# Kernel tuning notes

Measured on AMD Instinct MI355X. Metric: run time of the kernel, lower is better.

Reference implementation:

```python
import math
import jax, jax.numpy as jnp
import numpy as np
from jax import lax

FS = 16000.0
TAU_FAST_MS = 2.0
TAU_SLOW_MS = 60.0
EPS = 1e-6


def setup_inputs() -> dict:
    key = jax.random.key(0)
    B, C, T = 8, 64, 64000
    x = jax.random.normal(key, (B, C, T), dtype=jnp.float32)
    mu_fast = jnp.float32(1.0 - math.exp(-1.0 / (FS * TAU_FAST_MS / 1000.0)))
    mu_slow = jnp.float32(1.0 - math.exp(-1.0 / (FS * TAU_SLOW_MS / 1000.0)))
    mix_weight_adapt = jnp.float32(0.5)
    mix_weight_hp = jnp.float32(0.3)
    return {
        "x": x,
        "mu_fast": mu_fast,
        "mu_slow": mu_slow,
        "mix_weight_adapt": mix_weight_adapt,
        "mix_weight_hp": mix_weight_hp,
    }


def reference(x, mu_fast, mu_slow, mix_weight_adapt, mix_weight_hp):
    # x: [B, C, T]
    x = jnp.maximum(x, 0.0)
    xt = jnp.moveaxis(x, -1, 0)  # [T, B, C], time-leading for scan

    def step(carry, xcur):
        mf, ms = carry
        mf = (1.0 - mu_fast) * mf + mu_fast * xcur
        ms = (1.0 - mu_slow) * ms + mu_slow * xcur
        return (mf, ms), (mf, ms)

    init = (xt[0], xt[0])  # EMA initialized at first sample
    _, (mf_rest, ms_rest) = lax.scan(step, init, xt[1:])
    M_fast = jnp.concatenate([xt[:1], mf_rest], axis=0)  # [T, B, C]
    M_slow = jnp.concatenate([xt[:1], ms_rest], axis=0)

    mix_adapt = jax.nn.sigmoid(mix_weight_adapt)
    M = mix_adapt * M_fast + (1.0 - mix_adapt) * M_slow
    M = jnp.moveaxis(M, 0, -1)  # back to [B, C, T]

    x_adapted = x / (EPS + M)
    x_hp = x - M
    mix_hp = jax.nn.sigmoid(mix_weight_hp)
    return x_adapted + mix_hp * x_hp
```

## Files before the change

kernel.cpp:

```cpp
#include <hip/hip_runtime.h>


#define THREADS 128
#define WPB 2
#define K 25
#define WTILE (64 * K)
#define NBUF 3
#define T_LEN 64000
#define SEGS_W 4
#define SEG_LEN (T_LEN / SEGS_W)
#define SEG_TILES (SEG_LEN / WTILE)
#define HALO_TILES 4
#define EPS_V 1e-6f

typedef float nfloat4 __attribute__((ext_vector_type(4)));

__device__ __forceinline__ float rfl(float v) {
    return __int_as_float(__builtin_amdgcn_readfirstlane(__float_as_int(v)));
}

__device__ __forceinline__ void stage(const float* gt, float* b, int lane) {
#pragma unroll
    for (int c = 0; c < 6; ++c)
        __builtin_amdgcn_global_load_lds(
            (const __attribute__((address_space(1))) unsigned int*)(gt + c * 256 + lane * 4),
            (__attribute__((address_space(3))) unsigned int*)(b + c * 256),
            16, 0, 0);
    __builtin_amdgcn_global_load_lds(
        (const __attribute__((address_space(1))) unsigned int*)(gt + 1536 + lane),
        (__attribute__((address_space(3))) unsigned int*)(b + 1536),
        4, 0, 0);
}

__global__ __launch_bounds__(THREADS, 2)
void dual_ema_hp_kernel(const float* __restrict__ x,
                        const float* __restrict__ p_mu_fast,
                        const float* __restrict__ p_mu_slow,
                        const float* __restrict__ p_mwa,
                        const float* __restrict__ p_mhp,
                        float* __restrict__ out)
{
    __shared__ __align__(16) float lds[WPB * NBUF * WTILE];
    const int tid  = threadIdx.x;
    const int lane = tid & 63;
    const int wv   = tid >> 6;
    float* bufs = &lds[wv * NBUF * WTILE];

    const int gw  = blockIdx.x * WPB + wv;
    const int row = gw / SEGS_W;
    const int seg = gw % SEGS_W;
    const int h   = (seg == 0) ? 0 : HALO_TILES;
    const int nt  = SEG_TILES + h;

    const float* gseg = x   + (size_t)row * T_LEN + (size_t)seg * SEG_LEN - (size_t)h * WTILE;
    float*       oseg = out + (size_t)row * T_LEN + (size_t)seg * SEG_LEN - (size_t)h * WTILE;

    const float mu_f = rfl(p_mu_fast[0]);
    const float mu_s = rfl(p_mu_slow[0]);
    const float af = rfl(1.0f - mu_f);
    const float as = rfl(1.0f - mu_s);
    const float wa  = rfl(1.0f / (1.0f + __expf(-p_mwa[0])));
    const float wb  = rfl(1.0f - wa);
    const float whp = rfl(1.0f / (1.0f + __expf(-p_mhp[0])));

    const float Pf1  = rfl(__powf(af, (float)K));
    const float Ps1  = rfl(__powf(as, (float)K));
    const float Pf2  = rfl(Pf1 * Pf1),   Ps2  = rfl(Ps1 * Ps1);
    const float Pf4  = rfl(Pf2 * Pf2),   Ps4  = rfl(Ps2 * Ps2);
    const float Pf8  = rfl(Pf4 * Pf4),   Ps8  = rfl(Ps4 * Ps4);
    const float Pf16 = rfl(Pf8 * Pf8),   Ps16 = rfl(Ps8 * Ps8);
    const float Pf32 = rfl(Pf16 * Pf16), Ps32 = rfl(Ps16 * Ps16);

    stage(gseg,         bufs + 0 * WTILE, lane);
    stage(gseg + WTILE, bufs + 1 * WTILE, lane);

    float sfr = 0.0f, ssr = 0.0f;

    for (int t = 0; t < nt; ++t) {
        float* buf = bufs + (t % NBUF) * WTILE;

        if (t > h && t < nt - 1) { asm volatile("s_waitcnt vmcnt(14)" ::: "memory"); }
        else                     { asm volatile("s_waitcnt vmcnt(7)"  ::: "memory"); }

        if (t + 2 < nt)
            stage(gseg + (size_t)(t + 2) * WTILE, bufs + ((t + 2) % NBUF) * WTILE, lane);

        if (seg == 0 && t == 0 && lane == 0) {
            float y0 = fmaxf(buf[0], 0.0f);
            sfr = y0; ssr = y0;
        }

        float inf = (lane == 0) ? sfr : 0.0f;
        float ins = (lane == 0) ? ssr : 0.0f;
        float mf, ms;
        {
            float yv = fmaxf(buf[lane * K], 0.0f);
            mf = fmaf(af, inf, mu_f * yv);
            ms = fmaf(as, ins, mu_s * yv);
        }
#pragma unroll
        for (int i = 1; i < K; ++i) {
            float yv = fmaxf(buf[lane * K + i], 0.0f);
            mf = fmaf(af, mf, mu_f * yv);
            ms = fmaf(as, ms, mu_s * yv);
        }

        float cf = mf, cs = ms, uf, us;
        uf = __shfl_up(cf, 1);  us = __shfl_up(cs, 1);
        cf = (lane >= 1)  ? fmaf(Pf1,  uf, cf) : cf;  cs = (lane >= 1)  ? fmaf(Ps1,  us, cs) : cs;
        uf = __shfl_up(cf, 2);  us = __shfl_up(cs, 2);
        cf = (lane >= 2)  ? fmaf(Pf2,  uf, cf) : cf;  cs = (lane >= 2)  ? fmaf(Ps2,  us, cs) : cs;
        uf = __shfl_up(cf, 4);  us = __shfl_up(cs, 4);
        cf = (lane >= 4)  ? fmaf(Pf4,  uf, cf) : cf;  cs = (lane >= 4)  ? fmaf(Ps4,  us, cs) : cs;
        uf = __shfl_up(cf, 8);  us = __shfl_up(cs, 8);
        cf = (lane >= 8)  ? fmaf(Pf8,  uf, cf) : cf;  cs = (lane >= 8)  ? fmaf(Ps8,  us, cs) : cs;
        uf = __shfl_up(cf, 16); us = __shfl_up(cs, 16);
        cf = (lane >= 16) ? fmaf(Pf16, uf, cf) : cf;  cs = (lane >= 16) ? fmaf(Ps16, us, cs) : cs;
        uf = __shfl_up(cf, 32); us = __shfl_up(cs, 32);
        cf = (lane >= 32) ? fmaf(Pf32, uf, cf) : cf;  cs = (lane >= 32) ? fmaf(Ps32, us, cs) : cs;

        float ex_f = __shfl_up(cf, 1), ex_s = __shfl_up(cs, 1);
        if (lane == 0) { ex_f = sfr; ex_s = ssr; }
        sfr = __shfl(cf, 63);
        ssr = __shfl(cs, 63);

        asm volatile("s_waitcnt lgkmcnt(0)" ::: "memory");

        const bool emit = (t >= h);
        if (emit) {
            float mf2 = ex_f, ms2 = ex_s;
#pragma unroll
            for (int i = 0; i < K; ++i) {
                float yv = fmaxf(buf[lane * K + i], 0.0f);
                mf2 = fmaf(af, mf2, mu_f * yv);
                ms2 = fmaf(as, ms2, mu_s * yv);
                float M = fmaf(wa, mf2, wb * ms2);
                float o = yv * __builtin_amdgcn_rcpf(EPS_V + M) + whp * (yv - M);
                buf[lane * K + i] = o;
            }
            asm volatile("s_waitcnt lgkmcnt(0)" ::: "memory");

            float* gout = oseg + (size_t)t * WTILE;
            nfloat4* go4 = (nfloat4*)gout;
            const nfloat4* o4 = (const nfloat4*)buf;
#pragma unroll
            for (int c = 0; c < 6; ++c) {
                nfloat4 v = o4[c * 64 + lane];
                __builtin_nontemporal_store(v, &go4[c * 64 + lane]);
            }
            __builtin_nontemporal_store(buf[1536 + lane], &gout[1536 + lane]);
        }
    }
}

extern "C" void kernel_launch(void* const* d_in, const int* in_sizes, int n_in,
                              void* d_out, int out_size, void* d_ws, size_t ws_size,
                              hipStream_t stream) {
    const float* x    = (const float*)d_in[0];
    const float* mu_f = (const float*)d_in[1];
    const float* mu_s = (const float*)d_in[2];
    const float* mwa  = (const float*)d_in[3];
    const float* mhp  = (const float*)d_in[4];
    float* out = (float*)d_out;

    const int rows   = in_sizes[0] / T_LEN;
    const int blocks = rows * SEGS_W / WPB;
    dual_ema_hp_kernel<<<blocks, THREADS, 0, stream>>>(x, mu_f, mu_s, mwa, mhp, out);
}
```

Before: 249.5 us.

## Replace LDS-staged tiles with register-prefetched float4 scan over more segments

The LDS triple-buffer staging via global_load_lds is removed. Each lane now holds 4 consecutive samples in registers, and a 5-deep rotating register prefetch loads vectorised float4 directly from global memory. The wave scan now runs per 256-sample tile, and rows are split into 10 segments with a 25-tile halo, giving more waves and 256-thread blocks. This cuts LDS traffic and serial per-lane work and raises parallelism, at the cost of one shuffle scan per 256 samples instead of per 1600 and more redundant halo reads.

```diff
diff --git a/kernel.cpp b/kernel.cpp
--- a/kernel.cpp
+++ b/kernel.cpp
@@ -1,16 +1,15 @@
 #include <hip/hip_runtime.h>
 
 
-#define THREADS 128
-#define WPB 2
-#define K 25
-#define WTILE (64 * K)
-#define NBUF 3
+#define THREADS 256
+#define WPB 4
+#define MTILE 256
 #define T_LEN 64000
-#define SEGS_W 4
+#define SEGS_W 10
 #define SEG_LEN (T_LEN / SEGS_W)
-#define SEG_TILES (SEG_LEN / WTILE)
-#define HALO_TILES 4
+#define SEG_MT (SEG_LEN / MTILE)
+#define HALO_MT 25
+#define D 5
 #define EPS_V 1e-6f
 
 typedef float nfloat4 __attribute__((ext_vector_type(4)));
@@ -19,20 +18,7 @@
     return __int_as_float(__builtin_amdgcn_readfirstlane(__float_as_int(v)));
 }
 
-__device__ __forceinline__ void stage(const float* gt, float* b, int lane) {
-#pragma unroll
-    for (int c = 0; c < 6; ++c)
-        __builtin_amdgcn_global_load_lds(
-            (const __attribute__((address_space(1))) unsigned int*)(gt + c * 256 + lane * 4),
-            (__attribute__((address_space(3))) unsigned int*)(b + c * 256),
-            16, 0, 0);
-    __builtin_amdgcn_global_load_lds(
-        (const __attribute__((address_space(1))) unsigned int*)(gt + 1536 + lane),
-        (__attribute__((address_space(3))) unsigned int*)(b + 1536),
-        4, 0, 0);
-}
-
-__global__ __launch_bounds__(THREADS, 2)
+__global__ __launch_bounds__(THREADS, 5)
 void dual_ema_hp_kernel(const float* __restrict__ x,
                         const float* __restrict__ p_mu_fast,
                         const float* __restrict__ p_mu_slow,
@@ -40,20 +26,20 @@
                         const float* __restrict__ p_mhp,
                         float* __restrict__ out)
 {
-    __shared__ __align__(16) float lds[WPB * NBUF * WTILE];
     const int tid  = threadIdx.x;
     const int lane = tid & 63;
     const int wv   = tid >> 6;
-    float* bufs = &lds[wv * NBUF * WTILE];
 
     const int gw  = blockIdx.x * WPB + wv;
     const int row = gw / SEGS_W;
     const int seg = gw % SEGS_W;
-    const int h   = (seg == 0) ? 0 : HALO_TILES;
-    const int nt  = SEG_TILES + h;
+    const int h   = (seg == 0) ? 0 : HALO_MT;
+    const int total = SEG_MT + h;
 
-    const float* gseg = x   + (size_t)row * T_LEN + (size_t)seg * SEG_LEN - (size_t)h * WTILE;
-    float*       oseg = out + (size_t)row * T_LEN + (size_t)seg * SEG_LEN - (size_t)h * WTILE;
+    const float* gseg = x   + (size_t)row * T_LEN + (size_t)seg * SEG_LEN - (size_t)h * MTILE;
+    float*       oseg = out + (size_t)row * T_LEN + (size_t)seg * SEG_LEN - (size_t)h * MTILE;
+    const nfloat4* g4 = (const nfloat4*)gseg;
+    nfloat4*      go4 = (nfloat4*)oseg;
 
     const float mu_f = rfl(p_mu_fast[0]);
     const float mu_s = rfl(p_mu_slow[0]);
@@ -63,94 +49,82 @@
     const float wb  = rfl(1.0f - wa);
     const float whp = rfl(1.0f / (1.0f + __expf(-p_mhp[0])));
 
-    const float Pf1  = rfl(__powf(af, (float)K));
-    const float Ps1  = rfl(__powf(as, (float)K));
-    const float Pf2  = rfl(Pf1 * Pf1),   Ps2  = rfl(Ps1 * Ps1);
-    const float Pf4  = rfl(Pf2 * Pf2),   Ps4  = rfl(Ps2 * Ps2);
-    const float Pf8  = rfl(Pf4 * Pf4),   Ps8  = rfl(Ps4 * Ps4);
-    const float Pf16 = rfl(Pf8 * Pf8),   Ps16 = rfl(Ps8 * Ps8);
-    const float Pf32 = rfl(Pf16 * Pf16), Ps32 = rfl(Ps16 * Ps16);
-
-    stage(gseg,         bufs + 0 * WTILE, lane);
-    stage(gseg + WTILE, bufs + 1 * WTILE, lane);
+    const float af2 = af * af,  as2 = as * as;
+    const float Pf1  = rfl(af2 * af2),      Ps1  = rfl(as2 * as2);
+    const float Pf2  = rfl(Pf1 * Pf1),      Ps2  = rfl(Ps1 * Ps1);
+    const float Pf4  = rfl(Pf2 * Pf2),      Ps4  = rfl(Ps2 * Ps2);
+    const float Pf8  = rfl(Pf4 * Pf4),      Ps8  = rfl(Ps4 * Ps4);
+    const float Pf16 = rfl(Pf8 * Pf8),      Ps16 = rfl(Ps8 * Ps8);
+    const float Pf32 = rfl(Pf16 * Pf16),    Ps32 = rfl(Ps16 * Ps16);
 
     float sfr = 0.0f, ssr = 0.0f;
 
-    for (int t = 0; t < nt; ++t) {
-        float* buf = bufs + (t % NBUF) * WTILE;
+    nfloat4 r0 = g4[0 * 64 + lane];
+    nfloat4 r1 = g4[1 * 64 + lane];
+    nfloat4 r2 = g4[2 * 64 + lane];
+    nfloat4 r3 = g4[3 * 64 + lane];
+    nfloat4 r4 = g4[4 * 64 + lane];
 
-        if (t > h && t < nt - 1) { asm volatile("s_waitcnt vmcnt(14)" ::: "memory"); }
-        else                     { asm volatile("s_waitcnt vmcnt(7)"  ::: "memory"); }
+#define BODY(T_, RB_) do {                                                        \
+    nfloat4 v = RB_;                                                              \
+    if ((T_) + D < total) RB_ = g4[((T_) + D) * 64 + lane];                       \
+    float y0 = fmaxf(v.x, 0.0f), y1 = fmaxf(v.y, 0.0f);                           \
+    float y2 = fmaxf(v.z, 0.0f), y3 = fmaxf(v.w, 0.0f);                           \
+    if (seg == 0 && (T_) == 0 && lane == 0) { sfr = y0; ssr = y0; }               \
+    float inf = (lane == 0) ? sfr : 0.0f;                                         \
+    float ins = (lane == 0) ? ssr : 0.0f;                                         \
+    float mf = fmaf(af, inf, mu_f * y0);  float ms = fmaf(as, ins, mu_s * y0);    \
+    mf = fmaf(af, mf, mu_f * y1);         ms = fmaf(as, ms, mu_s * y1);           \
+    mf = fmaf(af, mf, mu_f * y2);         ms = fmaf(as, ms, mu_s * y2);           \
+    mf = fmaf(af, mf, mu_f * y3);         ms = fmaf(as, ms, mu_s * y3);           \
+    float cf = mf, cs = ms, uf, us;                                               \
+    uf = __shfl_up(cf, 1);  us = __shfl_up(cs, 1);                                \
+    cf = (lane >= 1)  ? fmaf(Pf1,  uf, cf) : cf;                                  \
+    cs = (lane >= 1)  ? fmaf(Ps1,  us, cs) : cs;                                  \
+    uf = __shfl_up(cf, 2);  us = __shfl_up(cs, 2);                                \
+    cf = (lane >= 2)  ? fmaf(Pf2,  uf, cf) : cf;                                  \
+    cs = (lane >= 2)  ? fmaf(Ps2,  us, cs) : cs;                                  \
+    uf = __shfl_up(cf, 4);  us = __shfl_up(cs, 4);                                \
+    cf = (lane >= 4)  ? fmaf(Pf4,  uf, cf) : cf;                                  \
+    cs = (lane >= 4)  ? fmaf(Ps4,  us, cs) : cs;                                  \
+    uf = __shfl_up(cf, 8);  us = __shfl_up(cs, 8);                                \
+    cf = (lane >= 8)  ? fmaf(Pf8,  uf, cf) : cf;                                  \
+    cs = (lane >= 8)  ? fmaf(Ps8,  us, cs) : cs;                                  \
+    uf = __shfl_up(cf, 16); us = __shfl_up(cs, 16);                               \
+    cf = (lane >= 16) ? fmaf(Pf16, uf, cf) : cf;                                  \
+    cs = (lane >= 16) ? fmaf(Ps16, us, cs) : cs;                                  \
+    uf = __shfl_up(cf, 32); us = __shfl_up(cs, 32);                               \
+    cf = (lane >= 32) ? fmaf(Pf32, uf, cf) : cf;                                  \
+    cs = (lane >= 32) ? fmaf(Ps32, us, cs) : cs;                                  \
+    float ex_f = __shfl_up(cf, 1), ex_s = __shfl_up(cs, 1);                       \
+    if (lane == 0) { ex_f = sfr; ex_s = ssr; }                                    \
+    sfr = __shfl(cf, 63); ssr = __shfl(cs, 63);                                   \
+    if ((T_) >= h) {                                                              \
+        float mf2 = ex_f, ms2 = ex_s; nfloat4 o;                                  \
+        mf2 = fmaf(af, mf2, mu_f * y0); ms2 = fmaf(as, ms2, mu_s * y0);           \
+        { float M = fmaf(wa, mf2, wb * ms2);                                      \
+          o.x = y0 * __builtin_amdgcn_rcpf(EPS_V + M) + whp * (y0 - M); }         \
+        mf2 = fmaf(af, mf2, mu_f * y1); ms2 = fmaf(as, ms2, mu_s * y1);           \
+        { float M = fmaf(wa, mf2, wb * ms2);                                      \
+          o.y = y1 * __builtin_amdgcn_rcpf(EPS_V + M) + whp * (y1 - M); }         \
+        mf2 = fmaf(af, mf2, mu_f * y2); ms2 = fmaf(as, ms2, mu_s * y2);           \
+        { float M = fmaf(wa, mf2, wb * ms2);                                      \
+          o.z = y2 * __builtin_amdgcn_rcpf(EPS_V + M) + whp * (y2 - M); }         \
+        mf2 = fmaf(af, mf2, mu_f * y3); ms2 = fmaf(as, ms2, mu_s * y3);           \
+        { float M = fmaf(wa, mf2, wb * ms2);                                      \
+          o.w = y3 * __builtin_amdgcn_rcpf(EPS_V + M) + whp * (y3 - M); }         \
+        __builtin_nontemporal_store(o, &go4[(T_) * 64 + lane]);                   \
+    }                                                                             \
+} while (0)
 
-        if (t + 2 < nt)
-            stage(gseg + (size_t)(t + 2) * WTILE, bufs + ((t + 2) % NBUF) * WTILE, lane);
-
-        if (seg == 0 && t == 0 && lane == 0) {
-            float y0 = fmaxf(buf[0], 0.0f);
-            sfr = y0; ssr = y0;
-        }
-
-        float inf = (lane == 0) ? sfr : 0.0f;
-        float ins = (lane == 0) ? ssr : 0.0f;
-        float mf, ms;
-        {
-            float yv = fmaxf(buf[lane * K], 0.0f);
-            mf = fmaf(af, inf, mu_f * yv);
-            ms = fmaf(as, ins, mu_s * yv);
-        }
-#pragma unroll
-        for (int i = 1; i < K; ++i) {
-            float yv = fmaxf(buf[lane * K + i], 0.0f);
-            mf = fmaf(af, mf, mu_f * yv);
-            ms = fmaf(as, ms, mu_s * yv);
-        }
-
-        float cf = mf, cs = ms, uf, us;
-        uf = __shfl_up(cf, 1);  us = __shfl_up(cs, 1);
-        cf = (lane >= 1)  ? fmaf(Pf1,  uf, cf) : cf;  cs = (lane >= 1)  ? fmaf(Ps1,  us, cs) : cs;
-        uf = __shfl_up(cf, 2);  us = __shfl_up(cs, 2);
-        cf = (lane >= 2)  ? fmaf(Pf2,  uf, cf) : cf;  cs = (lane >= 2)  ? fmaf(Ps2,  us, cs) : cs;
-        uf = __shfl_up(cf, 4);  us = __shfl_up(cs, 4);
-        cf = (lane >= 4)  ? fmaf(Pf4,  uf, cf) : cf;  cs = (lane >= 4)  ? fmaf(Ps4,  us, cs) : cs;
-        uf = __shfl_up(cf, 8);  us = __shfl_up(cs, 8);
-        cf = (lane >= 8)  ? fmaf(Pf8,  uf, cf) : cf;  cs = (lane >= 8)  ? fmaf(Ps8,  us, cs) : cs;
-        uf = __shfl_up(cf, 16); us = __shfl_up(cs, 16);
-        cf = (lane >= 16) ? fmaf(Pf16, uf, cf) : cf;  cs = (lane >= 16) ? fmaf(Ps16, us, cs) : cs;
-        uf = __shfl_up(cf, 32); us = __shfl_up(cs, 32);
-        cf = (lane >= 32) ? fmaf(Pf32, uf, cf) : cf;  cs = (lane >= 32) ? fmaf(Ps32, us, cs) : cs;
-
-        float ex_f = __shfl_up(cf, 1), ex_s = __shfl_up(cs, 1);
-        if (lane == 0) { ex_f = sfr; ex_s = ssr; }
-        sfr = __shfl(cf, 63);
-        ssr = __shfl(cs, 63);
-
-        asm volatile("s_waitcnt lgkmcnt(0)" ::: "memory");
-
-        const bool emit = (t >= h);
-        if (emit) {
-            float mf2 = ex_f, ms2 = ex_s;
-#pragma unroll
-            for (int i = 0; i < K; ++i) {
-                float yv = fmaxf(buf[lane * K + i], 0.0f);
-                mf2 = fmaf(af, mf2, mu_f * yv);
-                ms2 = fmaf(as, ms2, mu_s * yv);
-                float M = fmaf(wa, mf2, wb * ms2);
-                float o = yv * __builtin_amdgcn_rcpf(EPS_V + M) + whp * (yv - M);
-                buf[lane * K + i] = o;
-            }
-            asm volatile("s_waitcnt lgkmcnt(0)" ::: "memory");
-
-            float* gout = oseg + (size_t)t * WTILE;
-            nfloat4* go4 = (nfloat4*)gout;
-            const nfloat4* o4 = (const nfloat4*)buf;
-#pragma unroll
-            for (int c = 0; c < 6; ++c) {
-                nfloat4 v = o4[c * 64 + lane];
-                __builtin_nontemporal_store(v, &go4[c * 64 + lane]);
-            }
-            __builtin_nontemporal_store(buf[1536 + lane], &gout[1536 + lane]);
-        }
+    for (int tb = 0; tb < total; tb += D) {
+        BODY(tb + 0, r0);
+        BODY(tb + 1, r1);
+        BODY(tb + 2, r2);
+        BODY(tb + 3, r3);
+        BODY(tb + 4, r4);
     }
+#undef BODY
 }
 
 extern "C" void kernel_launch(void* const* d_in, const int* in_sizes, int n_in,
```

New measurement: 255.8 us. +2.5%, slower.
